# Kernel tuning notes

Hardware: AMD Instinct MI355X
Metric: run time of the kernel (lower is better)

## Reference

```python
import jax, jax.numpy as jnp
import numpy as np

H = 16          # num heads
HD = 64         # head dim
TEMPERATURE = 1.0
LN_EPS = 1e-5

def setup_inputs() -> dict:
    key = jax.random.key(0)
    ks = jax.random.split(key, 5)
    B, S, D = 2, 2048, 1024
    s = 1.0 / np.sqrt(D)
    return {
        "x": jax.random.normal(ks[0], (B, S, D), jnp.float32),
        "Wq": jax.random.normal(ks[1], (D, D), jnp.float32) * s,
        "bq": jnp.zeros((D,), jnp.float32),
        "Wk": jax.random.normal(ks[2], (D, D), jnp.float32) * s,
        "bk": jnp.zeros((D,), jnp.float32),
        "Wv": jax.random.normal(ks[3], (D, D), jnp.float32) * s,
        "bv": jnp.zeros((D,), jnp.float32),
        "Wo": jax.random.normal(ks[4], (D, D), jnp.float32) * s,
        "bo": jnp.zeros((D,), jnp.float32),
        "ln_gamma": jnp.ones((D,), jnp.float32),
        "ln_beta": jnp.zeros((D,), jnp.float32),
    }

def reference(x, Wq, bq, Wk, bk, Wv, bv, Wo, bo, ln_gamma, ln_beta):
    B, S, D = x.shape
    # LayerNorm (pre-attention)
    mu = jnp.mean(x, axis=-1, keepdims=True)
    var = jnp.mean(jnp.square(x - mu), axis=-1, keepdims=True)
    xn = (x - mu) * jax.lax.rsqrt(var + LN_EPS) * ln_gamma + ln_beta
    # Fused QKV projections (equivalent to H per-head Linears concatenated)
    q = (xn @ Wq + bq).reshape(B, S, H, HD)
    k = (xn @ Wk + bk).reshape(B, S, H, HD)
    v = (xn @ Wv + bv).reshape(B, S, H, HD)
    scale = np.sqrt(HD) * TEMPERATURE
    scores = jnp.einsum("bqhd,bkhd->bhqk", q, k) / scale
    attn = jax.nn.softmax(scores, axis=-1)  # dropout p=0 -> identity
    ctx = jnp.einsum("bhqk,bkhd->bqhd", attn, v).reshape(B, S, D)
    out = ctx @ Wo + bo
    return x + out
```

## Files before the change

### kernel.cpp

```cpp
#include <hip/hip_runtime.h>
#include <hip/hip_bf16.h>

#define Bc   2
#define Sc   2048
#define Dc   1024
#define Hc   16
#define HDc  64
#define MR   (Bc * Sc)
#define TBK  32
#define LOG2E 1.44269504088896f

typedef __attribute__((ext_vector_type(8))) short bf16x8;
typedef __attribute__((ext_vector_type(4))) float f32x4;

__device__ __forceinline__ unsigned short f2bf(float f) {
    __hip_bfloat16 h = __float2bfloat16(f);
    return *reinterpret_cast<unsigned short*>(&h);
}

__device__ __forceinline__ void gll16(const unsigned short* g, unsigned short* l) {
    __builtin_amdgcn_global_load_lds(
        (__attribute__((address_space(1))) const unsigned int*)g,
        (__attribute__((address_space(3))) unsigned int*)l,
        16, 0, 0);
}

__global__ __launch_bounds__(256) void prep_kernel(
        const float* __restrict__ x, const float* __restrict__ gamma,
        const float* __restrict__ beta, unsigned short* __restrict__ xn,
        const float* __restrict__ W0, const float* __restrict__ W1,
        const float* __restrict__ W2, const float* __restrict__ W3,
        unsigned short* __restrict__ T0, unsigned short* __restrict__ T1,
        unsigned short* __restrict__ T2, unsigned short* __restrict__ T3) {
    __shared__ float tile[64][65];
    int idx = blockIdx.x;
    int t = threadIdx.x;

    if (idx < 1024) {
        int z = idx >> 8, rem = idx & 255;
        const float* W = (z == 0) ? W0 : (z == 1) ? W1 : (z == 2) ? W2 : W3;
        unsigned short* T = (z == 0) ? T0 : (z == 1) ? T1 : (z == 2) ? T2 : T3;
        int nb = (rem & 15) * 64, kb = (rem >> 4) * 64;
        int r0 = t >> 4, c4 = (t & 15) * 4;
        #pragma unroll
        for (int rr = 0; rr < 4; rr++) {
            int row = rr * 16 + r0;
            float4 v = *(const float4*)(W + (size_t)(kb + row) * Dc + nb + c4);
            tile[row][c4 + 0] = v.x; tile[row][c4 + 1] = v.y;
            tile[row][c4 + 2] = v.z; tile[row][c4 + 3] = v.w;
        }
        __syncthreads();
        #pragma unroll
        for (int rr = 0; rr < 4; rr++) {
            int nrow = rr * 16 + r0;
            ushort4 o;
            o.x = f2bf(tile[c4 + 0][nrow]); o.y = f2bf(tile[c4 + 1][nrow]);
            o.z = f2bf(tile[c4 + 2][nrow]); o.w = f2bf(tile[c4 + 3][nrow]);
            *(ushort4*)(T + (size_t)(nb + nrow) * Dc + kb + c4) = o;
        }
    } else {
        int row = idx - 1024;
        const float4* xr = (const float4*)(x + (size_t)row * Dc);
        float4 v = xr[t];
        float s  = v.x + v.y + v.z + v.w;
        float ss = v.x * v.x + v.y * v.y + v.z * v.z + v.w * v.w;
        #pragma unroll
        for (int off = 32; off; off >>= 1) {
            s  += __shfl_xor(s, off, 64);
            ss += __shfl_xor(ss, off, 64);
        }
        float* red = tile[0];
        int w = t >> 6, lane = t & 63;
        if (lane == 0) { red[w * 2] = s; red[w * 2 + 1] = ss; }
        __syncthreads();
        s  = red[0] + red[2] + red[4] + red[6];
        ss = red[1] + red[3] + red[5] + red[7];
        float mean = s * (1.0f / Dc);
        float var  = ss * (1.0f / Dc) - mean * mean;
        float rstd = rsqrtf(var + 1e-5f);
        float4 g = ((const float4*)gamma)[t], bb = ((const float4*)beta)[t];
        ushort4 o;
        o.x = f2bf((v.x - mean) * rstd * g.x + bb.x);
        o.y = f2bf((v.y - mean) * rstd * g.y + bb.y);
        o.z = f2bf((v.z - mean) * rstd * g.z + bb.z);
        o.w = f2bf((v.w - mean) * rstd * g.w + bb.w);
        *(ushort4*)(xn + (size_t)row * Dc + t * 4) = o;
    }
}

__device__ __forceinline__ void gemm_core(const unsigned short* __restrict__ A,
                                          const unsigned short* __restrict__ Wt,
                                          unsigned short* As, unsigned short* Bs,
                                          int m0, int n0, f32x4 acc[4][4]) {
    int t = threadIdx.x;
    int w = t >> 6, lane = t & 63;
    int l16 = lane & 15, quad = lane >> 4;
    int wm = (w >> 1) * 64, wn = (w & 1) * 64;

    int srow = lane >> 2;
    int scol = (lane & 3) * 8;
    const unsigned short* Ag = A  + (size_t)(m0 + w * 16 + srow) * Dc + scol;
    const unsigned short* Bg = Wt + (size_t)(n0 + w * 16 + srow) * Dc + scol;
    unsigned short* Asw = As + (w * 16) * TBK;
    unsigned short* Bsw = Bs + (w * 16) * TBK;

    for (int k0 = 0; k0 < Dc; k0 += TBK) {
        gll16(Ag + k0, Asw);
        gll16(Ag + k0 + (size_t)64 * Dc, Asw + 64 * TBK);
        gll16(Bg + k0, Bsw);
        gll16(Bg + k0 + (size_t)64 * Dc, Bsw + 64 * TBK);
        __syncthreads();
        bf16x8 af[4], bfr[4];
        #pragma unroll
        for (int i = 0; i < 4; i++) {
            af[i]  = *(const bf16x8*)(As + (wm + i * 16 + l16) * TBK + quad * 8);
            bfr[i] = *(const bf16x8*)(Bs + (wn + i * 16 + l16) * TBK + quad * 8);
        }
        #pragma unroll
        for (int i = 0; i < 4; i++)
            #pragma unroll
            for (int j = 0; j < 4; j++)
                acc[i][j] = __builtin_amdgcn_mfma_f32_16x16x32_bf16(af[i], bfr[j], acc[i][j], 0, 0, 0);
        __syncthreads();
    }
}

__global__ __launch_bounds__(256) void gemm_qkv_kernel(
        const unsigned short* __restrict__ A,
        const unsigned short* __restrict__ Wqt, const unsigned short* __restrict__ Wkt,
        const unsigned short* __restrict__ Wvt,
        const float* __restrict__ bq, const float* __restrict__ bk,
        const float* __restrict__ bv,
        unsigned short* __restrict__ Qb, unsigned short* __restrict__ Kb,
        unsigned short* __restrict__ Vtb) {
    __shared__ unsigned short As[128 * TBK];
    __shared__ unsigned short Bs[128 * TBK];
    int z = blockIdx.z;
    const unsigned short* Wt = (z == 0) ? Wqt : (z == 1) ? Wkt : Wvt;
    const float* bias = (z == 0) ? bq : (z == 1) ? bk : bv;
    unsigned short* Out = (z == 0) ? Qb : (z == 1) ? Kb : Vtb;
    float outscale = (z == 0) ? (0.125f * LOG2E) : 1.0f;

    int n0 = blockIdx.x * 128, m0 = blockIdx.y * 128;
    f32x4 acc[4][4];
    #pragma unroll
    for (int i = 0; i < 4; i++)
        #pragma unroll
        for (int j = 0; j < 4; j++) acc[i][j] = (f32x4){0.f, 0.f, 0.f, 0.f};

    gemm_core(A, Wt, As, Bs, m0, n0, acc);

    int t = threadIdx.x;
    int w = t >> 6, lane = t & 63;
    int l16 = lane & 15, quad = lane >> 4;
    int wm = (w >> 1) * 64, wn = (w & 1) * 64;
    int b = m0 >> 11;
    #pragma unroll
    for (int j = 0; j < 4; j++) {
        int col = n0 + wn + j * 16 + l16;
        float bb = bias[col];
        int h = col >> 6, d = col & 63;
        #pragma unroll
        for (int i = 0; i < 4; i++) {
            #pragma unroll
            for (int r = 0; r < 4; r++) {
                int row = m0 + wm + i * 16 + quad * 4 + r;
                int s = row & (Sc - 1);
                unsigned short v = f2bf((acc[i][j][r] + bb) * outscale);
                if (z != 2)
                    Out[(((size_t)(b * Hc + h)) * Sc + s) * HDc + d] = v;
                else
                    Out[(((size_t)(b * Hc + h)) * HDc + d) * Sc + s] = v;
            }
        }
    }
}

__global__ __launch_bounds__(256) void gemm_o_kernel(
        const unsigned short* __restrict__ A,
        const unsigned short* __restrict__ Wot,
        const float* __restrict__ bo, const float* __restrict__ resid,
        float* __restrict__ Out) {
    __shared__ unsigned short As[64 * TBK];
    __shared__ unsigned short Bs[128 * TBK];
    int t = threadIdx.x;
    int w = t >> 6, lane = t & 63;
    int l16 = lane & 15, quad = lane >> 4;
    int wm = (w >> 1) * 32, wn = (w & 1) * 64;
    int n0 = blockIdx.x * 128, m0 = blockIdx.y * 64;

    f32x4 acc[2][4];
    #pragma unroll
    for (int i = 0; i < 2; i++)
        #pragma unroll
        for (int j = 0; j < 4; j++) acc[i][j] = (f32x4){0.f, 0.f, 0.f, 0.f};

    int srow = lane >> 2;
    int scol = (lane & 3) * 8;
    const unsigned short* Ag = A   + (size_t)(m0 + w * 16 + srow) * Dc + scol;
    const unsigned short* Bg = Wot + (size_t)(n0 + w * 16 + srow) * Dc + scol;
    unsigned short* Asw = As + (w * 16) * TBK;
    unsigned short* Bsw = Bs + (w * 16) * TBK;

    for (int k0 = 0; k0 < Dc; k0 += TBK) {
        gll16(Ag + k0, Asw);
        gll16(Bg + k0, Bsw);
        gll16(Bg + k0 + (size_t)64 * Dc, Bsw + 64 * TBK);
        __syncthreads();
        bf16x8 af[2], bfr[4];
        #pragma unroll
        for (int i = 0; i < 2; i++)
            af[i]  = *(const bf16x8*)(As + (wm + i * 16 + l16) * TBK + quad * 8);
        #pragma unroll
        for (int j = 0; j < 4; j++)
            bfr[j] = *(const bf16x8*)(Bs + (wn + j * 16 + l16) * TBK + quad * 8);
        #pragma unroll
        for (int i = 0; i < 2; i++)
            #pragma unroll
            for (int j = 0; j < 4; j++)
                acc[i][j] = __builtin_amdgcn_mfma_f32_16x16x32_bf16(af[i], bfr[j], acc[i][j], 0, 0, 0);
        __syncthreads();
    }

    #pragma unroll
    for (int j = 0; j < 4; j++) {
        int col = n0 + wn + j * 16 + l16;
        float bb = bo[col];
        #pragma unroll
        for (int i = 0; i < 2; i++) {
            #pragma unroll
            for (int r = 0; r < 4; r++) {
                int row = m0 + wm + i * 16 + quad * 4 + r;
                size_t off = (size_t)row * Dc + col;
                Out[off] = acc[i][j][r] + bb + resid[off];
            }
        }
    }
}

#define BKa 64
#define LDP 72

__global__ __launch_bounds__(256, 2) void attn_mfma_kernel(
        const unsigned short* __restrict__ Q,
        const unsigned short* __restrict__ K,
        const unsigned short* __restrict__ Vt,
        unsigned short* __restrict__ O) {
    __shared__ unsigned short Ks[BKa * LDP];
    __shared__ unsigned short Vs[HDc * LDP];
    __shared__ unsigned short Ps[4 * 32 * LDP];

    int t = threadIdx.x;
    int w = t >> 6, lane = t & 63;
    int quad = lane >> 4, l16 = lane & 15;
    int q0 = blockIdx.x * 128;
    int bh = blockIdx.y;
    size_t qkbase = (size_t)bh * Sc * HDc;
    size_t vbase  = (size_t)bh * HDc * Sc;

    bf16x8 qf[2][2];
    #pragma unroll
    for (int jq = 0; jq < 2; jq++) {
        const unsigned short* qr = Q + qkbase
            + (size_t)(q0 + w * 32 + jq * 16 + l16) * HDc + quad * 8;
        qf[jq][0] = *(const bf16x8*)(qr);
        qf[jq][1] = *(const bf16x8*)(qr + 32);
    }

    f32x4 Oacc[2][4];
    #pragma unroll
    for (int jq = 0; jq < 2; jq++)
        #pragma unroll
        for (int n = 0; n < 4; n++) Oacc[jq][n] = (f32x4){0.f, 0.f, 0.f, 0.f};
    float lacc[2] = {0.f, 0.f};

    int srow = t >> 2, sseg = t & 3;
    const unsigned short* Kg = K + qkbase + (size_t)srow * HDc + sseg * 16;
    const unsigned short* Vg = Vt + vbase + (size_t)srow * Sc + sseg * 16;
    unsigned short* pw = Ps + w * 32 * LDP;
    unsigned short* ksw = Ks + srow * LDP + sseg * 16;
    unsigned short* vsw = Vs + srow * LDP + sseg * 16;
    const int NT = Sc / BKa;

    bf16x8 kv0 = *(const bf16x8*)(Kg);
    bf16x8 kv1 = *(const bf16x8*)(Kg + 8);
    bf16x8 vv0 = *(const bf16x8*)(Vg);
    bf16x8 vv1 = *(const bf16x8*)(Vg + 8);

    for (int kt = 0; kt < NT; kt++) {
        __syncthreads();
        *(bf16x8*)(ksw)     = kv0;
        *(bf16x8*)(ksw + 8) = kv1;
        *(bf16x8*)(vsw)     = vv0;
        *(bf16x8*)(vsw + 8) = vv1;
        __syncthreads();

        int ktn = (kt + 1 < NT) ? kt + 1 : kt;
        const unsigned short* kgn = Kg + (size_t)ktn * BKa * HDc;
        const unsigned short* vgn = Vg + ktn * BKa;
        kv0 = *(const bf16x8*)(kgn);
        kv1 = *(const bf16x8*)(kgn + 8);
        vv0 = *(const bf16x8*)(vgn);
        vv1 = *(const bf16x8*)(vgn + 8);

        f32x4 st[2][4];
        #pragma unroll
        for (int m = 0; m < 4; m++) {
            const unsigned short* kb = Ks + (m * 16 + l16) * LDP + quad * 8;
            bf16x8 kf0 = *(const bf16x8*)(kb);
            bf16x8 kf1 = *(const bf16x8*)(kb + 32);
            #pragma unroll
            for (int jq = 0; jq < 2; jq++) {
                f32x4 s = (f32x4){0.f, 0.f, 0.f, 0.f};
                s = __builtin_amdgcn_mfma_f32_16x16x32_bf16(kf0, qf[jq][0], s, 0, 0, 0);
                s = __builtin_amdgcn_mfma_f32_16x16x32_bf16(kf1, qf[jq][1], s, 0, 0, 0);
                st[jq][m] = s;
            }
        }

        #pragma unroll
        for (int jq = 0; jq < 2; jq++) {
            #pragma unroll
            for (int m = 0; m < 4; m++) {
                float p0 = __builtin_amdgcn_exp2f(st[jq][m][0]);
                float p1 = __builtin_amdgcn_exp2f(st[jq][m][1]);
                float p2 = __builtin_amdgcn_exp2f(st[jq][m][2]);
                float p3 = __builtin_amdgcn_exp2f(st[jq][m][3]);
                lacc[jq] += (p0 + p1) + (p2 + p3);
                ushort4 pk;
                pk.x = f2bf(p0); pk.y = f2bf(p1); pk.z = f2bf(p2); pk.w = f2bf(p3);
                *(ushort4*)(pw + (jq * 16 + l16) * LDP + m * 16 + quad * 4) = pk;
            }
        }

        #pragma unroll
        for (int kk = 0; kk < 2; kk++) {
            bf16x8 vf[4];
            #pragma unroll
            for (int n = 0; n < 4; n++)
                vf[n] = *(const bf16x8*)(Vs + (n * 16 + l16) * LDP + kk * 32 + quad * 8);
            #pragma unroll
            for (int jq = 0; jq < 2; jq++) {
                bf16x8 pf = *(const bf16x8*)(pw + (jq * 16 + l16) * LDP + kk * 32 + quad * 8);
                #pragma unroll
                for (int n = 0; n < 4; n++)
                    Oacc[jq][n] = __builtin_amdgcn_mfma_f32_16x16x32_bf16(pf, vf[n], Oacc[jq][n], 0, 0, 0);
            }
        }
    }

    int b = bh >> 4, h = bh & 15;
    #pragma unroll
    for (int jq = 0; jq < 2; jq++) {
        lacc[jq] += __shfl_xor(lacc[jq], 16, 64);
        lacc[jq] += __shfl_xor(lacc[jq], 32, 64);
        #pragma unroll
        for (int i = 0; i < 4; i++) {
            float li = __shfl(lacc[jq], quad * 4 + i, 64);
            float rl = 1.0f / li;
            int q = q0 + w * 32 + jq * 16 + quad * 4 + i;
            #pragma unroll
            for (int n = 0; n < 4; n++) {
                O[((size_t)(b * Sc + q)) * Dc + h * HDc + n * 16 + l16] =
                    f2bf(Oacc[jq][n][i] * rl);
            }
        }
    }
}

extern "C" void kernel_launch(void* const* d_in, const int* in_sizes, int n_in,
                              void* d_out, int out_size, void* d_ws, size_t ws_size,
                              hipStream_t stream) {
    const float* x     = (const float*)d_in[0];
    const float* Wq    = (const float*)d_in[1];
    const float* bq    = (const float*)d_in[2];
    const float* Wk    = (const float*)d_in[3];
    const float* bk    = (const float*)d_in[4];
    const float* Wv    = (const float*)d_in[5];
    const float* bv    = (const float*)d_in[6];
    const float* Wo    = (const float*)d_in[7];
    const float* bo    = (const float*)d_in[8];
    const float* gamma = (const float*)d_in[9];
    const float* beta  = (const float*)d_in[10];
    float* out = (float*)d_out;

    unsigned short* us = (unsigned short*)d_ws;
    const size_t NE = (size_t)MR * Dc;
    const size_t WE = (size_t)Dc * Dc;
    unsigned short* xn  = us;
    unsigned short* Qb  = us + NE;
    unsigned short* Kb  = us + 2 * NE;
    unsigned short* Vtb = us + 3 * NE;
    unsigned short* ctx = us + 4 * NE;
    unsigned short* Wqt = us + 5 * NE;
    unsigned short* Wkt = Wqt + WE;
    unsigned short* Wvt = Wkt + WE;
    unsigned short* Wot = Wvt + WE;

    prep_kernel<<<1024 + MR, 256, 0, stream>>>(x, gamma, beta, xn,
                                               Wq, Wk, Wv, Wo,
                                               Wqt, Wkt, Wvt, Wot);

    dim3 qkvgrid(Dc / 128, MR / 128, 3);
    gemm_qkv_kernel<<<qkvgrid, 256, 0, stream>>>(xn, Wqt, Wkt, Wvt, bq, bk, bv,
                                                 Qb, Kb, Vtb);

    dim3 agrid(Sc / 128, Bc * Hc);
    attn_mfma_kernel<<<agrid, 256, 0, stream>>>(Qb, Kb, Vtb, ctx);

    dim3 ogrid(Dc / 128, MR / 64);
    gemm_o_kernel<<<ogrid, 256, 0, stream>>>(ctx, Wot, bo, x, out);
}
```

Baseline: 200.3 us.

## Load K/V fragments directly from global, drop LDS staging and remap block order

The attention kernel stops staging K and V tiles in shared memory. Each wave now loads its MFMA fragments straight from global memory (relying on L2/L1 hits), which removes the two block-wide barriers per key tile. Block indices are remapped so consecutive blocks cover different batch-heads at the same query tile, changing which blocks run together and share cache. The cost is four times the global/L1 traffic, because every wave reloads the same K/V. Loads also become exposed latency with no explicit prefetch into the next tile.

```diff
diff --git a/kernel.cpp b/kernel.cpp
--- a/kernel.cpp
+++ b/kernel.cpp
@@ -246,15 +246,15 @@
         const unsigned short* __restrict__ K,
         const unsigned short* __restrict__ Vt,
         unsigned short* __restrict__ O) {
-    __shared__ unsigned short Ks[BKa * LDP];
-    __shared__ unsigned short Vs[HDc * LDP];
     __shared__ unsigned short Ps[4 * 32 * LDP];
 
     int t = threadIdx.x;
     int w = t >> 6, lane = t & 63;
     int quad = lane >> 4, l16 = lane & 15;
-    int q0 = blockIdx.x * 128;
-    int bh = blockIdx.y;
+
+    int bid = blockIdx.x + gridDim.x * blockIdx.y;
+    int q0 = (bid >> 5) * 128;
+    int bh = bid & 31;
     size_t qkbase = (size_t)bh * Sc * HDc;
     size_t vbase  = (size_t)bh * HDc * Sc;
 
@@ -274,46 +274,36 @@
         for (int n = 0; n < 4; n++) Oacc[jq][n] = (f32x4){0.f, 0.f, 0.f, 0.f};
     float lacc[2] = {0.f, 0.f};
 
-    int srow = t >> 2, sseg = t & 3;
-    const unsigned short* Kg = K + qkbase + (size_t)srow * HDc + sseg * 16;
-    const unsigned short* Vg = Vt + vbase + (size_t)srow * Sc + sseg * 16;
     unsigned short* pw = Ps + w * 32 * LDP;
-    unsigned short* ksw = Ks + srow * LDP + sseg * 16;
-    unsigned short* vsw = Vs + srow * LDP + sseg * 16;
+    const unsigned short* Kg = K + qkbase;
+    const unsigned short* Vg = Vt + vbase;
     const int NT = Sc / BKa;
 
-    bf16x8 kv0 = *(const bf16x8*)(Kg);
-    bf16x8 kv1 = *(const bf16x8*)(Kg + 8);
-    bf16x8 vv0 = *(const bf16x8*)(Vg);
-    bf16x8 vv1 = *(const bf16x8*)(Vg + 8);
-
     for (int kt = 0; kt < NT; kt++) {
-        __syncthreads();
-        *(bf16x8*)(ksw)     = kv0;
-        *(bf16x8*)(ksw + 8) = kv1;
-        *(bf16x8*)(vsw)     = vv0;
-        *(bf16x8*)(vsw + 8) = vv1;
-        __syncthreads();
-
-        int ktn = (kt + 1 < NT) ? kt + 1 : kt;
-        const unsigned short* kgn = Kg + (size_t)ktn * BKa * HDc;
-        const unsigned short* vgn = Vg + ktn * BKa;
-        kv0 = *(const bf16x8*)(kgn);
-        kv1 = *(const bf16x8*)(kgn + 8);
-        vv0 = *(const bf16x8*)(vgn);
-        vv1 = *(const bf16x8*)(vgn + 8);
+        bf16x8 kf[4][2];
+        #pragma unroll
+        for (int m = 0; m < 4; m++) {
+            const unsigned short* kp = Kg
+                + (size_t)(kt * BKa + m * 16 + l16) * HDc + quad * 8;
+            kf[m][0] = *(const bf16x8*)(kp);
+            kf[m][1] = *(const bf16x8*)(kp + 32);
+        }
+        bf16x8 vf[2][4];
+        #pragma unroll
+        for (int kk = 0; kk < 2; kk++)
+            #pragma unroll
+            for (int n = 0; n < 4; n++)
+                vf[kk][n] = *(const bf16x8*)(Vg
+                    + (size_t)(n * 16 + l16) * Sc + kt * BKa + kk * 32 + quad * 8);
 
         f32x4 st[2][4];
         #pragma unroll
         for (int m = 0; m < 4; m++) {
-            const unsigned short* kb = Ks + (m * 16 + l16) * LDP + quad * 8;
-            bf16x8 kf0 = *(const bf16x8*)(kb);
-            bf16x8 kf1 = *(const bf16x8*)(kb + 32);
             #pragma unroll
             for (int jq = 0; jq < 2; jq++) {
                 f32x4 s = (f32x4){0.f, 0.f, 0.f, 0.f};
-                s = __builtin_amdgcn_mfma_f32_16x16x32_bf16(kf0, qf[jq][0], s, 0, 0, 0);
-                s = __builtin_amdgcn_mfma_f32_16x16x32_bf16(kf1, qf[jq][1], s, 0, 0, 0);
+                s = __builtin_amdgcn_mfma_f32_16x16x32_bf16(kf[m][0], qf[jq][0], s, 0, 0, 0);
+                s = __builtin_amdgcn_mfma_f32_16x16x32_bf16(kf[m][1], qf[jq][1], s, 0, 0, 0);
                 st[jq][m] = s;
             }
         }
@@ -335,16 +325,12 @@
 
         #pragma unroll
         for (int kk = 0; kk < 2; kk++) {
-            bf16x8 vf[4];
-            #pragma unroll
-            for (int n = 0; n < 4; n++)
-                vf[n] = *(const bf16x8*)(Vs + (n * 16 + l16) * LDP + kk * 32 + quad * 8);
             #pragma unroll
             for (int jq = 0; jq < 2; jq++) {
                 bf16x8 pf = *(const bf16x8*)(pw + (jq * 16 + l16) * LDP + kk * 32 + quad * 8);
                 #pragma unroll
                 for (int n = 0; n < 4; n++)
-                    Oacc[jq][n] = __builtin_amdgcn_mfma_f32_16x16x32_bf16(pf, vf[n], Oacc[jq][n], 0, 0, 0);
+                    Oacc[jq][n] = __builtin_amdgcn_mfma_f32_16x16x32_bf16(pf, vf[kk][n], Oacc[jq][n], 0, 0, 0);
             }
         }
     }
```

After: 269.2 us. +34.4%, slower.

## Swizzle attention LDS tiles, remap block order, add MFMA priority hints

Applied to the files above, without the earlier changes.

Replaces the padded LDS layout (row stride 72) with an unpadded 64-wide layout using an XOR swizzle of 16-byte chunks by row index for the K, V and P tiles. This aims to avoid bank conflicts while cutting LDS footprint. It also remaps the block index so consecutive blocks cover different batch-heads of the same query tile. It raises wave priority around the MFMA sections with s_setprio. The swizzle must stay consistent between writes and reads, and the block remap changes cache locality for K/V reuse.

```diff
diff --git a/kernel.cpp b/kernel.cpp
--- a/kernel.cpp
+++ b/kernel.cpp
@@ -239,22 +239,23 @@
 }
 
 #define BKa 64
-#define LDP 72
 
 __global__ __launch_bounds__(256, 2) void attn_mfma_kernel(
         const unsigned short* __restrict__ Q,
         const unsigned short* __restrict__ K,
         const unsigned short* __restrict__ Vt,
         unsigned short* __restrict__ O) {
-    __shared__ unsigned short Ks[BKa * LDP];
-    __shared__ unsigned short Vs[HDc * LDP];
-    __shared__ unsigned short Ps[4 * 32 * LDP];
+    __shared__ unsigned short Ks[BKa * 64];
+    __shared__ unsigned short Vs[HDc * 64];
+    __shared__ unsigned short Ps[4 * 32 * 64];
 
     int t = threadIdx.x;
     int w = t >> 6, lane = t & 63;
     int quad = lane >> 4, l16 = lane & 15;
-    int q0 = blockIdx.x * 128;
-    int bh = blockIdx.y;
+
+    int bid = blockIdx.x + gridDim.x * blockIdx.y;
+    int q0 = (bid >> 5) * 128;
+    int bh = bid & 31;
     size_t qkbase = (size_t)bh * Sc * HDc;
     size_t vbase  = (size_t)bh * HDc * Sc;
 
@@ -277,9 +278,13 @@
     int srow = t >> 2, sseg = t & 3;
     const unsigned short* Kg = K + qkbase + (size_t)srow * HDc + sseg * 16;
     const unsigned short* Vg = Vt + vbase + (size_t)srow * Sc + sseg * 16;
-    unsigned short* pw = Ps + w * 32 * LDP;
-    unsigned short* ksw = Ks + srow * LDP + sseg * 16;
-    unsigned short* vsw = Vs + srow * LDP + sseg * 16;
+    unsigned short* pw = Ps + w * 32 * 64;
+    int rm_w = srow & 7;
+    unsigned short* ksw0 = Ks + srow * 64 + ((2 * sseg)     ^ rm_w) * 8;
+    unsigned short* ksw1 = Ks + srow * 64 + ((2 * sseg + 1) ^ rm_w) * 8;
+    unsigned short* vsw0 = Vs + srow * 64 + ((2 * sseg)     ^ rm_w) * 8;
+    unsigned short* vsw1 = Vs + srow * 64 + ((2 * sseg + 1) ^ rm_w) * 8;
+    int rm = l16 & 7;
     const int NT = Sc / BKa;
 
     bf16x8 kv0 = *(const bf16x8*)(Kg);
@@ -289,10 +294,10 @@
 
     for (int kt = 0; kt < NT; kt++) {
         __syncthreads();
-        *(bf16x8*)(ksw)     = kv0;
-        *(bf16x8*)(ksw + 8) = kv1;
-        *(bf16x8*)(vsw)     = vv0;
-        *(bf16x8*)(vsw + 8) = vv1;
+        *(bf16x8*)(ksw0) = kv0;
+        *(bf16x8*)(ksw1) = kv1;
+        *(bf16x8*)(vsw0) = vv0;
+        *(bf16x8*)(vsw1) = vv1;
         __syncthreads();
 
         int ktn = (kt + 1 < NT) ? kt + 1 : kt;
@@ -304,11 +309,12 @@
         vv1 = *(const bf16x8*)(vgn + 8);
 
         f32x4 st[2][4];
+        __builtin_amdgcn_s_setprio(1);
         #pragma unroll
         for (int m = 0; m < 4; m++) {
-            const unsigned short* kb = Ks + (m * 16 + l16) * LDP + quad * 8;
-            bf16x8 kf0 = *(const bf16x8*)(kb);
-            bf16x8 kf1 = *(const bf16x8*)(kb + 32);
+            const unsigned short* kr = Ks + (m * 16 + l16) * 64;
+            bf16x8 kf0 = *(const bf16x8*)(kr + (quad       ^ rm) * 8);
+            bf16x8 kf1 = *(const bf16x8*)(kr + ((quad + 4) ^ rm) * 8);
             #pragma unroll
             for (int jq = 0; jq < 2; jq++) {
                 f32x4 s = (f32x4){0.f, 0.f, 0.f, 0.f};
@@ -317,9 +323,11 @@
                 st[jq][m] = s;
             }
         }
+        __builtin_amdgcn_s_setprio(0);
 
         #pragma unroll
         for (int jq = 0; jq < 2; jq++) {
+            unsigned short* pr = pw + (jq * 16 + l16) * 64;
             #pragma unroll
             for (int m = 0; m < 4; m++) {
                 float p0 = __builtin_amdgcn_exp2f(st[jq][m][0]);
@@ -329,24 +337,28 @@
                 lacc[jq] += (p0 + p1) + (p2 + p3);
                 ushort4 pk;
                 pk.x = f2bf(p0); pk.y = f2bf(p1); pk.z = f2bf(p2); pk.w = f2bf(p3);
-                *(ushort4*)(pw + (jq * 16 + l16) * LDP + m * 16 + quad * 4) = pk;
-            }
-        }
-
+                *(ushort4*)(pr + ((2 * m + (quad >> 1)) ^ rm) * 8 + (quad & 1) * 4) = pk;
+            }
+        }
+
+        __builtin_amdgcn_s_setprio(1);
         #pragma unroll
         for (int kk = 0; kk < 2; kk++) {
             bf16x8 vf[4];
             #pragma unroll
             for (int n = 0; n < 4; n++)
-                vf[n] = *(const bf16x8*)(Vs + (n * 16 + l16) * LDP + kk * 32 + quad * 8);
+                vf[n] = *(const bf16x8*)(Vs + (n * 16 + l16) * 64
+                                         + ((4 * kk + quad) ^ rm) * 8);
             #pragma unroll
             for (int jq = 0; jq < 2; jq++) {
-                bf16x8 pf = *(const bf16x8*)(pw + (jq * 16 + l16) * LDP + kk * 32 + quad * 8);
+                bf16x8 pf = *(const bf16x8*)(pw + (jq * 16 + l16) * 64
+                                             + ((4 * kk + quad) ^ rm) * 8);
                 #pragma unroll
                 for (int n = 0; n < 4; n++)
                     Oacc[jq][n] = __builtin_amdgcn_mfma_f32_16x16x32_bf16(pf, vf[n], Oacc[jq][n], 0, 0, 0);
             }
         }
+        __builtin_amdgcn_s_setprio(0);
     }
 
     int b = bh >> 4, h = bh & 15;
```

Result: faster. 195.5 us (-2.4%).
